# Performance work log

Measured on AMD Instinct MI355X. Metric: run time of the kernel, lower is better.

The kernel has to match this reference:

```python
import jax, jax.numpy as jnp
import numpy as np

N_NODES = 50000
EPS = 1e-12  # F.normalize eps


def _gcn_layer(x, W, b, src, dst):
    # GCNConv(normalize=False): h = x @ W, then sum-aggregate messages from
    # source nodes into target nodes along edge_index, then add bias.
    h = x @ W
    agg = jax.ops.segment_sum(h[src], dst, num_segments=N_NODES)
    out = agg + b
    # F.normalize(p=2, dim=-1) then ReLU
    norm = jnp.linalg.norm(out, axis=-1, keepdims=True)
    out = out / jnp.maximum(norm, EPS)
    return jax.nn.relu(out)


def setup_inputs() -> dict:
    key = jax.random.key(0)
    ks = jax.random.split(key, 8)
    nfeat, nhid, nclass, n_edges = 128, 128, 40, 640000
    x = jax.random.normal(ks[0], (N_NODES, nfeat), dtype=jnp.float32)
    edge_index = jax.random.randint(ks[1], (2, n_edges), 0, N_NODES, dtype=jnp.int64)
    s = 1.0 / np.sqrt(nhid)
    return {
        "x": x,
        "edge_index": edge_index,
        "W1": jax.random.normal(ks[2], (nfeat, nhid), jnp.float32) * s,
        "b1": jnp.zeros((nhid,), jnp.float32),
        "W2": jax.random.normal(ks[3], (nhid, nhid), jnp.float32) * s,
        "b2": jnp.zeros((nhid,), jnp.float32),
        "W3": jax.random.normal(ks[4], (nhid, nhid), jnp.float32) * s,
        "b3": jnp.zeros((nhid,), jnp.float32),
        "W4": jax.random.normal(ks[5], (nhid, nhid), jnp.float32) * s,
        "b4": jnp.zeros((nhid,), jnp.float32),
        "Wl": jax.random.normal(ks[6], (nhid, nclass), jnp.float32) * s,
        "bl": jnp.zeros((nclass,), jnp.float32),
    }


def reference(x, edge_index, W1, b1, W2, b2, W3, b3, W4, b4, Wl, bl):
    src, dst = edge_index[0], edge_index[1]
    x1 = _gcn_layer(x, W1, b1, src, dst)
    x2 = _gcn_layer(x1, W2, b2, src, dst)
    x3 = _gcn_layer(x2, W3, b3, src, dst)
    x4 = _gcn_layer(x3, W4, b4, src, dst)
    logits = x4 @ Wl + bl
    probs = jax.nn.softmax(logits, axis=-1)
    return (logits, probs, x4)
```

## Files before the change

### kernel.cpp

```cpp
#include <hip/hip_runtime.h>
#include <hip/hip_bf16.h>
#include <hip/hip_fp16.h>
#include <math.h>

#define NFEAT 128
#define NCLASS 40

typedef __attribute__((ext_vector_type(8))) short frag_ab;
typedef __attribute__((ext_vector_type(4))) float frag_cd;

static __device__ inline unsigned short f2bf_rne(float f) {
    union { float f; unsigned u; } v;
    v.f = f;
    unsigned r = v.u + 0x7FFFu + ((v.u >> 16) & 1u);
    return (unsigned short)(r >> 16);
}
static __device__ inline float bf2f(unsigned short h) {
    union { unsigned u; float f; } v;
    v.u = ((unsigned)h) << 16;
    return v.f;
}


__global__ __launch_bounds__(256) void prep_kernel(const float* __restrict__ x,
                                                   __half* __restrict__ xh, int xc4,
                                                   const float* __restrict__ W0,
                                                   const float* __restrict__ W1,
                                                   const float* __restrict__ W2,
                                                   const float* __restrict__ W3,
                                                   short* __restrict__ whi,
                                                   short* __restrict__ wlo,
                                                   const int* __restrict__ dst,
                                                   int* __restrict__ cnt, int n_edges,
                                                   int convB) {
    int b = blockIdx.x;
    if (b < convB) {
        int i = b * 256 + threadIdx.x;
        if (i < xc4) {
            float4 v = ((const float4*)x)[i];
            ((__half2*)xh)[i * 2 + 0] = __floats2half2_rn(v.x, v.y);
            ((__half2*)xh)[i * 2 + 1] = __floats2half2_rn(v.z, v.w);
        }
    } else if (b < convB + 32) {
        int wb = b - convB;
        int layer = wb >> 3;
        const float* W = layer == 0 ? W0 : layer == 1 ? W1 : layer == 2 ? W2 : W3;
        short* h = whi + (size_t)layer * 16384;
        short* l = wlo + (size_t)layer * 16384;
        int idx = (wb & 7) * 256 + threadIdx.x;
        int lane = idx & 63;
        int t = (idx >> 6) & 7;
        int s = idx >> 9;
        int quad = lane >> 4;
        int n = lane & 15;
        int kbase = s * 32 + quad * 8;
        int col = t * 16 + n;
#pragma unroll
        for (int j = 0; j < 8; ++j) {
            float f = W[(size_t)(kbase + j) * NFEAT + col];
            unsigned short hb = f2bf_rne(f);
            unsigned short lb = f2bf_rne(f - bf2f(hb));
            h[(size_t)idx * 8 + j] = (short)hb;
            l[(size_t)idx * 8 + j] = (short)lb;
        }
    } else {
        int hb = b - convB - 32;
        int i = hb * 256 + threadIdx.x;
        int n4 = n_edges >> 2;
        if (i < n4) {
            int4 d = ((const int4*)dst)[i];
            atomicAdd(&cnt[d.x], 1);
            atomicAdd(&cnt[d.y], 1);
            atomicAdd(&cnt[d.z], 1);
            atomicAdd(&cnt[d.w], 1);
        }
        if (hb == 0 && threadIdx.x == 0) {
            for (int e = n4 << 2; e < n_edges; ++e) atomicAdd(&cnt[dst[e]], 1);
        }
    }
}


__global__ __launch_bounds__(256) void scan1_kernel(const int* __restrict__ cnt,
                                                    int* __restrict__ excl,
                                                    int* __restrict__ bsums,
                                                    int* __restrict__ hist, int n) {
    __shared__ int sd[256];
    __shared__ int lh[64];
    int t = threadIdx.x;
    int i = blockIdx.x * 256 + t;
    if (t < 64) lh[t] = 0;
    int v = (i < n) ? cnt[i] : 0;
    sd[t] = v;
    __syncthreads();
#pragma unroll
    for (int off = 1; off < 256; off <<= 1) {
        int tmp = (t >= off) ? sd[t - off] : 0;
        __syncthreads();
        sd[t] += tmp;
        __syncthreads();
    }
    if (i < n) {
        excl[i] = sd[t] - v;
        atomicAdd(&lh[v < 63 ? v : 63], 1);
    }
    if (t == 255) bsums[blockIdx.x] = sd[255];
    __syncthreads();
    if (t < 64 && lh[t]) atomicAdd(&hist[t], lh[t]);
}

__global__ __launch_bounds__(256) void scan3_kernel(const int* __restrict__ excl,
                                                    const int* __restrict__ bsums,
                                                    int* __restrict__ row_ptr,
                                                    int* __restrict__ woff,
                                                    const int* __restrict__ cnt,
                                                    const int* __restrict__ hist,
                                                    int* __restrict__ hoff,
                                                    int* __restrict__ perm,
                                                    int n, int nb) {
    __shared__ int sd[256];
    __shared__ int off_s, tot_s;
    __shared__ int hincl[64];
    __shared__ int bcnt[64];
    __shared__ int bbase[64];
    int t = threadIdx.x;
    if (t < 64) bcnt[t] = 0;
    int v = (t < nb) ? bsums[t] : 0;
    sd[t] = v;
    __syncthreads();
#pragma unroll
    for (int off = 1; off < 256; off <<= 1) {
        int tmp = (t >= off) ? sd[t - off] : 0;
        __syncthreads();
        sd[t] += tmp;
        __syncthreads();
    }
    if (t == 0) {
        off_s = (blockIdx.x > 0) ? sd[blockIdx.x - 1] : 0;
        tot_s = sd[255];
        int s = 0;
        for (int d = 0; d < 64; ++d) { s += hist[d]; hincl[d] = s; }
    }
    __syncthreads();
    int i = blockIdx.x * 256 + t;
    int d = 0, myslot = 0;
    if (i < n) {
        int val = excl[i] + off_s;
        row_ptr[i] = val;
        woff[i] = val;
        int deg = cnt[i];
        d = deg < 63 ? deg : 63;
        myslot = atomicAdd(&bcnt[d], 1);
    }
    if (i == 0) row_ptr[n] = tot_s;
    __syncthreads();
    if (t < 64 && bcnt[t]) bbase[t] = atomicAdd(&hoff[t], bcnt[t]);
    __syncthreads();
    if (i < n) {
        perm[(n - hincl[d]) + bbase[d] + myslot] = i;
    }
}

__global__ __launch_bounds__(256) void scatter_kernel(const int* __restrict__ src,
                                                      const int* __restrict__ dst,
                                                      int* __restrict__ woff,
                                                      int* __restrict__ src_sorted, int n_edges) {
    int i = blockIdx.x * 256 + threadIdx.x;
    int n4 = n_edges >> 2;
    if (i < n4) {
        int4 d = ((const int4*)dst)[i];
        int4 s = ((const int4*)src)[i];
        int p0 = atomicAdd(&woff[d.x], 1);
        int p1 = atomicAdd(&woff[d.y], 1);
        int p2 = atomicAdd(&woff[d.z], 1);
        int p3 = atomicAdd(&woff[d.w], 1);
        src_sorted[p0] = s.x;
        src_sorted[p1] = s.y;
        src_sorted[p2] = s.z;
        src_sorted[p3] = s.w;
    }
    if (i == 0) {
        for (int e = n4 << 2; e < n_edges; ++e) {
            int p = atomicAdd(&woff[dst[e]], 1);
            src_sorted[p] = src[e];
        }
    }
}


__global__ __launch_bounds__(256) void gcn_fused_kernel(const __half* __restrict__ xin,
                                                        const int* __restrict__ row_ptr,
                                                        const int* __restrict__ src_sorted,
                                                        const int* __restrict__ perm,
                                                        const short* __restrict__ whi,
                                                        const short* __restrict__ wlo,
                                                        const float* __restrict__ bias,
                                                        float* __restrict__ outf,
                                                        __half* __restrict__ outh, int M) {
    __shared__ float smem[64][132];
    __shared__ int ctr;
    int tid = threadIdx.x;
    int base = blockIdx.x * 64;
    if (tid == 0) ctr = 0;
    __syncthreads();

    {
        int c = tid & 15;
        int lane = tid & 63;
        const uint4* xp = (const uint4*)xin;
        for (;;) {
            int nl = 0;
            if ((lane & 15) == 0) nl = atomicAdd(&ctr, 1);
            nl = __shfl(nl, lane & 48);
            if (nl >= 64) break;
            int slot = base + nl;
            float a[8];
#pragma unroll
            for (int i = 0; i < 8; ++i) a[i] = 0.f;
            int jb = 0, je = 0;
            if (slot < M) {
                int node = perm[slot];
                jb = row_ptr[node];
                je = row_ptr[node + 1];
            }

            int j = jb;
            int i0 = 0, i1 = 0, i2 = 0, i3 = 0;
            bool have4 = (j + 4 <= je);
            if (have4) {
                i0 = src_sorted[j];
                i1 = src_sorted[j + 1];
                i2 = src_sorted[j + 2];
                i3 = src_sorted[j + 3];
            }
            while (have4) {
                uint4 r0 = xp[i0 * 16 + c];
                uint4 r1 = xp[i1 * 16 + c];
                uint4 r2 = xp[i2 * 16 + c];
                uint4 r3 = xp[i3 * 16 + c];
                int jn = j + 4;
                bool more = (jn + 4 <= je);
                if (more) {
                    i0 = src_sorted[jn];
                    i1 = src_sorted[jn + 1];
                    i2 = src_sorted[jn + 2];
                    i3 = src_sorted[jn + 3];
                }
#pragma unroll
                for (int q = 0; q < 4; ++q) {
                    unsigned u0 = (&r0.x)[q], u1 = (&r1.x)[q], u2 = (&r2.x)[q], u3 = (&r3.x)[q];
                    float2 f0 = __half22float2(*(__half2*)&u0);
                    float2 f1 = __half22float2(*(__half2*)&u1);
                    float2 f2 = __half22float2(*(__half2*)&u2);
                    float2 f3 = __half22float2(*(__half2*)&u3);
                    a[q * 2 + 0] += f0.x + f1.x + f2.x + f3.x;
                    a[q * 2 + 1] += f0.y + f1.y + f2.y + f3.y;
                }
                j = jn;
                have4 = more;
            }
            for (; j < je; ++j) {
                int s0 = src_sorted[j];
                uint4 r0 = xp[s0 * 16 + c];
#pragma unroll
                for (int q = 0; q < 4; ++q) {
                    unsigned u0 = (&r0.x)[q];
                    float2 f0 = __half22float2(*(__half2*)&u0);
                    a[q * 2 + 0] += f0.x;
                    a[q * 2 + 1] += f0.y;
                }
            }
            float4* wp = (float4*)&smem[nl][c * 8];
            wp[0] = make_float4(a[0], a[1], a[2], a[3]);
            wp[1] = make_float4(a[4], a[5], a[6], a[7]);
        }
    }
    __syncthreads();

    int wave = tid >> 6;
    int lane = tid & 63;
    int quad = lane >> 4;
    int n16 = lane & 15;
    int lrow = wave * 16 + n16;

    const frag_ab* WH = (const frag_ab*)whi;
    const frag_ab* WL = (const frag_ab*)wlo;

    frag_cd acc[8];
#pragma unroll
    for (int t = 0; t < 8; ++t) acc[t] = (frag_cd){0.f, 0.f, 0.f, 0.f};

#pragma unroll
    for (int s = 0; s < 4; ++s) {
        const float* ap = &smem[lrow][s * 32 + quad * 8];
        float4 v0 = *(const float4*)(ap);
        float4 v1 = *(const float4*)(ap + 4);
        float fv[8] = {v0.x, v0.y, v0.z, v0.w, v1.x, v1.y, v1.z, v1.w};
        frag_ab ah, al;
#pragma unroll
        for (int jj = 0; jj < 8; ++jj) {
            unsigned short hb = f2bf_rne(fv[jj]);
            ah[jj] = (short)hb;
            al[jj] = (short)f2bf_rne(fv[jj] - bf2f(hb));
        }
#pragma unroll
        for (int t = 0; t < 8; ++t) {
            frag_ab bh = WH[(s * 8 + t) * 64 + lane];
            frag_ab bl = WL[(s * 8 + t) * 64 + lane];
            acc[t] = __builtin_amdgcn_mfma_f32_16x16x32_bf16(ah, bh, acc[t], 0, 0, 0);
            acc[t] = __builtin_amdgcn_mfma_f32_16x16x32_bf16(ah, bl, acc[t], 0, 0, 0);
            acc[t] = __builtin_amdgcn_mfma_f32_16x16x32_bf16(al, bh, acc[t], 0, 0, 0);
        }
    }

    float ssq[4] = {0.f, 0.f, 0.f, 0.f};
#pragma unroll
    for (int t = 0; t < 8; ++t) {
        float bv = bias[t * 16 + n16];
#pragma unroll
        for (int r = 0; r < 4; ++r) {
            acc[t][r] += bv;
            ssq[r] += acc[t][r] * acc[t][r];
        }
    }
#pragma unroll
    for (int mask = 1; mask <= 8; mask <<= 1) {
#pragma unroll
        for (int r = 0; r < 4; ++r) ssq[r] += __shfl_xor(ssq[r], mask);
    }
    float inv[4];
#pragma unroll
    for (int r = 0; r < 4; ++r) inv[r] = 1.0f / fmaxf(sqrtf(ssq[r]), 1e-12f);

    int slot0 = base + wave * 16 + quad * 4;
#pragma unroll
    for (int r = 0; r < 4; ++r) {
        int slot = slot0 + r;
        if (slot < M) {
            int orow = perm[slot];
            if (outh) {
                __half* op = outh + (size_t)orow * NFEAT + n16;
#pragma unroll
                for (int t = 0; t < 8; ++t)
                    op[t * 16] = __float2half(fmaxf(acc[t][r] * inv[r], 0.f));
            } else {
                float* op = outf + (size_t)orow * NFEAT + n16;
#pragma unroll
                for (int t = 0; t < 8; ++t)
                    op[t * 16] = fmaxf(acc[t][r] * inv[r], 0.f);
            }
        }
    }
}


__global__ __launch_bounds__(256) void classifier_kernel(const float* __restrict__ x4,
                                                         const float* __restrict__ Wl,
                                                         const float* __restrict__ bl,
                                                         float* __restrict__ logits,
                                                         float* __restrict__ probs, int n_nodes) {
    int node = blockIdx.x * 256 + threadIdx.x;
    int nc = node < n_nodes ? node : n_nodes - 1;
    const float* row = x4 + (size_t)nc * NFEAT;

    float acc[NCLASS];
#pragma unroll
    for (int c = 0; c < NCLASS; ++c) acc[c] = bl[c];

    for (int k = 0; k < NFEAT; k += 4) {
        float4 a = *(const float4*)(row + k);
#pragma unroll
        for (int kk = 0; kk < 4; ++kk) {
            float av = (&a.x)[kk];
            const float* Wr = Wl + (k + kk) * NCLASS;
#pragma unroll
            for (int c = 0; c < NCLASS; ++c) acc[c] += av * Wr[c];
        }
    }

    float m = acc[0];
#pragma unroll
    for (int c = 1; c < NCLASS; ++c) m = fmaxf(m, acc[c]);
    float ex[NCLASS];
    float sum = 0.f;
#pragma unroll
    for (int c = 0; c < NCLASS; ++c) {
        ex[c] = __expf(acc[c] - m);
        sum += ex[c];
    }
    float is = 1.0f / sum;

    if (node < n_nodes) {
        float4* lo = (float4*)(logits + (size_t)node * NCLASS);
        float4* po = (float4*)(probs + (size_t)node * NCLASS);
#pragma unroll
        for (int c = 0; c < NCLASS; c += 4) {
            float4 lv, pv;
            lv.x = acc[c + 0]; lv.y = acc[c + 1]; lv.z = acc[c + 2]; lv.w = acc[c + 3];
            pv.x = ex[c + 0] * is; pv.y = ex[c + 1] * is; pv.z = ex[c + 2] * is; pv.w = ex[c + 3] * is;
            lo[c >> 2] = lv;
            po[c >> 2] = pv;
        }
    }
}


extern "C" void kernel_launch(void* const* d_in, const int* in_sizes, int n_in,
                              void* d_out, int out_size, void* d_ws, size_t ws_size,
                              hipStream_t stream) {
    const float* x  = (const float*)d_in[0];
    const int*   ei = (const int*)d_in[1];
    const float* W1 = (const float*)d_in[2];
    const float* b1 = (const float*)d_in[3];
    const float* W2 = (const float*)d_in[4];
    const float* b2 = (const float*)d_in[5];
    const float* W3 = (const float*)d_in[6];
    const float* b3 = (const float*)d_in[7];
    const float* W4 = (const float*)d_in[8];
    const float* b4 = (const float*)d_in[9];
    const float* Wl = (const float*)d_in[10];
    const float* bl = (const float*)d_in[11];

    const int n_nodes = in_sizes[0] / NFEAT;
    const int n_edges = in_sizes[1] / 2;
    const int* src = ei;
    const int* dst = ei + n_edges;

    float* out    = (float*)d_out;
    float* logits = out;
    float* probs  = out + (size_t)n_nodes * NCLASS;
    float* x4     = out + 2 * (size_t)n_nodes * NCLASS;

    char* ws = (char*)d_ws;
    size_t off = 0;
    auto wsalloc = [&](size_t bytes) -> void* {
        void* p = ws + off;
        off += (bytes + 255) & ~(size_t)255;
        return p;
    };
    __half* xh         = (__half*)wsalloc((size_t)n_nodes * NFEAT * sizeof(__half));
    __half* xh2        = (__half*)wsalloc((size_t)n_nodes * NFEAT * sizeof(__half));
    int*    row_ptr    = (int*)wsalloc(((size_t)n_nodes + 1) * sizeof(int));
    int*    woff       = (int*)wsalloc((size_t)n_nodes * sizeof(int));
    int*    cnt        = (int*)wsalloc(((size_t)n_nodes + 128) * sizeof(int));
    int*    hist       = cnt + n_nodes;
    int*    hoff       = cnt + n_nodes + 64;
    int*    perm       = (int*)wsalloc((size_t)n_nodes * sizeof(int));
    int*    src_sorted = (int*)wsalloc((size_t)n_edges * sizeof(int));
    int     nbt        = (n_nodes + 255) / 256;
    int*    bsums      = (int*)wsalloc(((size_t)nbt + 1) * sizeof(int));
    short*  whi        = (short*)wsalloc((size_t)4 * 16384 * sizeof(short));
    short*  wlo        = (short*)wsalloc((size_t)4 * 16384 * sizeof(short));

    hipMemsetAsync(cnt, 0, ((size_t)n_nodes + 128) * sizeof(int), stream);

    int xc4   = (n_nodes * NFEAT) / 4;
    int convB = (xc4 + 255) / 256;
    int e4b   = ((n_edges >> 2) + 255) / 256;
    prep_kernel<<<convB + 32 + e4b, 256, 0, stream>>>(x, xh, xc4,
                                                      W1, W2, W3, W4, whi, wlo,
                                                      dst, cnt, n_edges, convB);

    scan1_kernel<<<nbt, 256, 0, stream>>>(cnt, row_ptr , bsums, hist, n_nodes);
    scan3_kernel<<<nbt, 256, 0, stream>>>(row_ptr, bsums, row_ptr, woff,
                                          cnt, hist, hoff, perm, n_nodes, nbt);
    scatter_kernel<<<e4b, 256, 0, stream>>>(src, dst, woff, src_sorted, n_edges);

    int gb = (n_nodes + 63) / 64;
    int cb = (n_nodes + 255) / 256;

    gcn_fused_kernel<<<gb, 256, 0, stream>>>(xh,  row_ptr, src_sorted, perm, whi + 0 * 16384, wlo + 0 * 16384, b1, nullptr, xh2, n_nodes);
    gcn_fused_kernel<<<gb, 256, 0, stream>>>(xh2, row_ptr, src_sorted, perm, whi + 1 * 16384, wlo + 1 * 16384, b2, nullptr, xh,  n_nodes);
    gcn_fused_kernel<<<gb, 256, 0, stream>>>(xh,  row_ptr, src_sorted, perm, whi + 2 * 16384, wlo + 2 * 16384, b3, nullptr, xh2, n_nodes);
    gcn_fused_kernel<<<gb, 256, 0, stream>>>(xh2, row_ptr, src_sorted, perm, whi + 3 * 16384, wlo + 3 * 16384, b4, x4, nullptr, n_nodes);

    classifier_kernel<<<cb, 256, 0, stream>>>(x4, Wl, bl, logits, probs, n_nodes);
}
```

Before: 348.8 us.

## Bucket CSR neighbor lists by source range for gather locality

Edges are counted and scattered per (source range, destination) bucket, with the range taken as src>>12 over 13 ranges, so each node's neighbor list is partially sorted by source index. The aim is better cache locality when the fused GCN layers gather source rows, across all four layers. The cost is 13x larger count and offset arrays, a bigger memset, and extra passes in the scan kernels.

```diff
diff --git a/kernel.cpp b/kernel.cpp
--- a/kernel.cpp
+++ b/kernel.cpp
@@ -5,6 +5,8 @@
 
 #define NFEAT 128
 #define NCLASS 40
+#define RSHIFT 12
+#define NRANGE 13
 
 typedef __attribute__((ext_vector_type(8))) short frag_ab;
 typedef __attribute__((ext_vector_type(4))) float frag_cd;
@@ -30,9 +32,10 @@
                                                    const float* __restrict__ W3,
                                                    short* __restrict__ whi,
                                                    short* __restrict__ wlo,
+                                                   const int* __restrict__ src,
                                                    const int* __restrict__ dst,
-                                                   int* __restrict__ cnt, int n_edges,
-                                                   int convB) {
+                                                   int* __restrict__ cntR, int n_nodes,
+                                                   int n_edges, int convB) {
     int b = blockIdx.x;
     if (b < convB) {
         int i = b * 256 + threadIdx.x;
@@ -69,19 +72,22 @@
         int n4 = n_edges >> 2;
         if (i < n4) {
             int4 d = ((const int4*)dst)[i];
-            atomicAdd(&cnt[d.x], 1);
-            atomicAdd(&cnt[d.y], 1);
-            atomicAdd(&cnt[d.z], 1);
-            atomicAdd(&cnt[d.w], 1);
+            int4 s = ((const int4*)src)[i];
+            atomicAdd(&cntR[(size_t)(s.x >> RSHIFT) * n_nodes + d.x], 1);
+            atomicAdd(&cntR[(size_t)(s.y >> RSHIFT) * n_nodes + d.y], 1);
+            atomicAdd(&cntR[(size_t)(s.z >> RSHIFT) * n_nodes + d.z], 1);
+            atomicAdd(&cntR[(size_t)(s.w >> RSHIFT) * n_nodes + d.w], 1);
         }
         if (hb == 0 && threadIdx.x == 0) {
-            for (int e = n4 << 2; e < n_edges; ++e) atomicAdd(&cnt[dst[e]], 1);
-        }
-    }
-}
-
-
-__global__ __launch_bounds__(256) void scan1_kernel(const int* __restrict__ cnt,
+            for (int e = n4 << 2; e < n_edges; ++e)
+                atomicAdd(&cntR[(size_t)(src[e] >> RSHIFT) * n_nodes + dst[e]], 1);
+        }
+    }
+}
+
+
+__global__ __launch_bounds__(256) void scan1_kernel(const int* __restrict__ cntR,
+                                                    int* __restrict__ cnt,
                                                     int* __restrict__ excl,
                                                     int* __restrict__ bsums,
                                                     int* __restrict__ hist, int n) {
@@ -90,7 +96,11 @@
     int t = threadIdx.x;
     int i = blockIdx.x * 256 + t;
     if (t < 64) lh[t] = 0;
-    int v = (i < n) ? cnt[i] : 0;
+    int v = 0;
+    if (i < n) {
+#pragma unroll
+        for (int r = 0; r < NRANGE; ++r) v += cntR[(size_t)r * n + i];
+    }
     sd[t] = v;
     __syncthreads();
 #pragma unroll
@@ -101,6 +111,7 @@
         __syncthreads();
     }
     if (i < n) {
+        cnt[i] = v;
         excl[i] = sd[t] - v;
         atomicAdd(&lh[v < 63 ? v : 63], 1);
     }
@@ -112,7 +123,8 @@
 __global__ __launch_bounds__(256) void scan3_kernel(const int* __restrict__ excl,
                                                     const int* __restrict__ bsums,
                                                     int* __restrict__ row_ptr,
-                                                    int* __restrict__ woff,
+                                                    const int* __restrict__ cntR,
+                                                    int* __restrict__ woffR,
                                                     const int* __restrict__ cnt,
                                                     const int* __restrict__ hist,
                                                     int* __restrict__ hoff,
@@ -147,7 +159,13 @@
     if (i < n) {
         int val = excl[i] + off_s;
         row_ptr[i] = val;
-        woff[i] = val;
+        int run = val;
+#pragma unroll
+        for (int r = 0; r < NRANGE; ++r) {
+            int c = cntR[(size_t)r * n + i];
+            woffR[(size_t)r * n + i] = run;
+            run += c;
+        }
         int deg = cnt[i];
         d = deg < 63 ? deg : 63;
         myslot = atomicAdd(&bcnt[d], 1);
@@ -163,17 +181,18 @@
 
 __global__ __launch_bounds__(256) void scatter_kernel(const int* __restrict__ src,
                                                       const int* __restrict__ dst,
-                                                      int* __restrict__ woff,
-                                                      int* __restrict__ src_sorted, int n_edges) {
+                                                      int* __restrict__ woffR,
+                                                      int* __restrict__ src_sorted,
+                                                      int n_nodes, int n_edges) {
     int i = blockIdx.x * 256 + threadIdx.x;
     int n4 = n_edges >> 2;
     if (i < n4) {
         int4 d = ((const int4*)dst)[i];
         int4 s = ((const int4*)src)[i];
-        int p0 = atomicAdd(&woff[d.x], 1);
-        int p1 = atomicAdd(&woff[d.y], 1);
-        int p2 = atomicAdd(&woff[d.z], 1);
-        int p3 = atomicAdd(&woff[d.w], 1);
+        int p0 = atomicAdd(&woffR[(size_t)(s.x >> RSHIFT) * n_nodes + d.x], 1);
+        int p1 = atomicAdd(&woffR[(size_t)(s.y >> RSHIFT) * n_nodes + d.y], 1);
+        int p2 = atomicAdd(&woffR[(size_t)(s.z >> RSHIFT) * n_nodes + d.z], 1);
+        int p3 = atomicAdd(&woffR[(size_t)(s.w >> RSHIFT) * n_nodes + d.w], 1);
         src_sorted[p0] = s.x;
         src_sorted[p1] = s.y;
         src_sorted[p2] = s.z;
@@ -181,7 +200,7 @@
     }
     if (i == 0) {
         for (int e = n4 << 2; e < n_edges; ++e) {
-            int p = atomicAdd(&woff[dst[e]], 1);
+            int p = atomicAdd(&woffR[(size_t)(src[e] >> RSHIFT) * n_nodes + dst[e]], 1);
             src_sorted[p] = src[e];
         }
     }
@@ -441,10 +460,11 @@
     __half* xh         = (__half*)wsalloc((size_t)n_nodes * NFEAT * sizeof(__half));
     __half* xh2        = (__half*)wsalloc((size_t)n_nodes * NFEAT * sizeof(__half));
     int*    row_ptr    = (int*)wsalloc(((size_t)n_nodes + 1) * sizeof(int));
-    int*    woff       = (int*)wsalloc((size_t)n_nodes * sizeof(int));
-    int*    cnt        = (int*)wsalloc(((size_t)n_nodes + 128) * sizeof(int));
-    int*    hist       = cnt + n_nodes;
-    int*    hoff       = cnt + n_nodes + 64;
+    int*    cntR       = (int*)wsalloc(((size_t)NRANGE * n_nodes + 128) * sizeof(int));
+    int*    hist       = cntR + (size_t)NRANGE * n_nodes;
+    int*    hoff       = hist + 64;
+    int*    woffR      = (int*)wsalloc((size_t)NRANGE * n_nodes * sizeof(int));
+    int*    cnt        = (int*)wsalloc((size_t)n_nodes * sizeof(int));
     int*    perm       = (int*)wsalloc((size_t)n_nodes * sizeof(int));
     int*    src_sorted = (int*)wsalloc((size_t)n_edges * sizeof(int));
     int     nbt        = (n_nodes + 255) / 256;
@@ -452,19 +472,20 @@
     short*  whi        = (short*)wsalloc((size_t)4 * 16384 * sizeof(short));
     short*  wlo        = (short*)wsalloc((size_t)4 * 16384 * sizeof(short));
 
-    hipMemsetAsync(cnt, 0, ((size_t)n_nodes + 128) * sizeof(int), stream);
+    hipMemsetAsync(cntR, 0, ((size_t)NRANGE * n_nodes + 128) * sizeof(int), stream);
 
     int xc4   = (n_nodes * NFEAT) / 4;
     int convB = (xc4 + 255) / 256;
     int e4b   = ((n_edges >> 2) + 255) / 256;
     prep_kernel<<<convB + 32 + e4b, 256, 0, stream>>>(x, xh, xc4,
                                                       W1, W2, W3, W4, whi, wlo,
-                                                      dst, cnt, n_edges, convB);
-
-    scan1_kernel<<<nbt, 256, 0, stream>>>(cnt, row_ptr , bsums, hist, n_nodes);
-    scan3_kernel<<<nbt, 256, 0, stream>>>(row_ptr, bsums, row_ptr, woff,
+                                                      src, dst, cntR, n_nodes,
+                                                      n_edges, convB);
+
+    scan1_kernel<<<nbt, 256, 0, stream>>>(cntR, cnt, row_ptr , bsums, hist, n_nodes);
+    scan3_kernel<<<nbt, 256, 0, stream>>>(row_ptr, bsums, row_ptr, cntR, woffR,
                                           cnt, hist, hoff, perm, n_nodes, nbt);
-    scatter_kernel<<<e4b, 256, 0, stream>>>(src, dst, woff, src_sorted, n_edges);
+    scatter_kernel<<<e4b, 256, 0, stream>>>(src, dst, woffR, src_sorted, n_nodes, n_edges);
 
     int gb = (n_nodes + 63) / 64;
     int cb = (n_nodes + 255) / 256;
```

Measured after the change: 348.1 us. Within noise of the previous version (-0.2%).
